# Optimization experiments

Measured on AMD Instinct MI355X. Metric: run time of the kernel, lower is better.

## Reference

```python
import jax, jax.numpy as jnp
import numpy as np

B, CI, CO = 8, 32, 32
M1, M2 = 16, 16
H, W = 128, 128
TOTAL = M1 + M2 + M1 * M2  # 288


def setup_inputs() -> dict:
    key = jax.random.key(0)
    k1, k2, k3 = jax.random.split(key, 3)
    scale = 1.0 / (CI * CO)
    x = jax.random.normal(k1, (B, CI, H, W), dtype=jnp.float32)
    weight_real = scale * jax.random.uniform(k2, (CI, CO, TOTAL), dtype=jnp.float32)
    weight_imag = scale * jax.random.uniform(k3, (CI, CO, TOTAL), dtype=jnp.float32)
    return {"x": x, "weight_real": weight_real, "weight_imag": weight_imag}


def reference(x, weight_real, weight_imag):
    w = (weight_real + 1j * weight_imag).astype(jnp.complex64)
    pole1 = w[:, :, :M1]                                   # [i,o,p]
    pole2 = w[:, :, M1:M1 + M2]                            # [i,o,q]
    residue = w[:, :, M1 + M2:].reshape(CI, CO, M1, M2)    # [i,o,p,q]

    Hh, Wd = x.shape[-2], x.shape[-1]
    ty = jnp.linspace(0.0, 1.0, Hh)   # grid along dim -2
    tx = jnp.linspace(0.0, 1.0, Wd)   # grid along dim -1
    dty = ty[1] - ty[0]
    dtx = tx[1] - tx[0]

    # FFT (torch default norm='backward': no scaling on forward)
    alpha = jnp.fft.fft2(x, axes=(-2, -1))[:, :, :M1, :M2]  # [b,i,f,g] complex

    lam1 = (jnp.fft.fftfreq(Hh, dty) * (2.0 * np.pi) * 1j)[:M1].astype(jnp.complex64)  # [f]
    lam2 = (jnp.fft.fftfreq(Wd, dtx) * (2.0 * np.pi) * 1j)[:M2].astype(jnp.complex64)  # [g]

    # pole-residue transfer function Hw[f,g,i,o,p,q] = res[i,o,p,q] / ((lam1[f]-pole1[i,o,p]) * (lam2[g]-pole2[i,o,q]))
    d1 = lam1[:, None, None, None] - pole1[None]  # [f,i,o,p]
    d2 = lam2[:, None, None, None] - pole2[None]  # [g,i,o,q]
    Hw = residue[None, None] / (d1[:, None, :, :, :, None] * d2[None, :, :, :, None, :])  # [f,g,i,o,p,q]

    # contractions matching torch einsums 'biox,oxikpq->bkox' and '->bkpq'
    or1 = jnp.einsum('bifg,fgiopq->bofg', alpha, Hw)  # [b,o,f,g]
    or2 = jnp.einsum('bifg,fgiopq->bopq', alpha, Hw)  # [b,o,p,q]

    # ifft2 with zero-padding of modes to full (H, W), norm='backward' (1/(HW) on inverse)
    x1 = jnp.real(jnp.fft.ifft2(or1, s=(Hh, Wd), axes=(-2, -1)))

    # time-domain pole exponentials
    e1 = jnp.exp(pole1[..., None] * ty.astype(jnp.complex64))  # [i,o,p,z]
    e2 = jnp.exp(pole2[..., None] * tx.astype(jnp.complex64))  # [i,o,q,x]
    # x2[b,o,z,x] = sum_{i,p,q} or2[b,o,p,q] e1[i,o,p,z] e2[i,o,q,x]  (avoids 6D [i,o,p,q,H,W] intermediate)
    tmp = jnp.einsum('bopq,iopz->bioqz', or2, e1)          # [b,i,o,q,z]
    x2 = jnp.real(jnp.einsum('bioqz,ioqx->bozx', tmp, e2)) / (Hh * Wd)

    return x1 + x2
```

## Files before the change

### kernel.cpp

```cpp
#include <hip/hip_runtime.h>

#define TOT 288
#define W1C 6.2340979026f
#define TWOPI_128 0.049087385212340517f

typedef short short8 __attribute__((ext_vector_type(8)));
typedef float f32x4 __attribute__((ext_vector_type(4)));
typedef unsigned short u16;
typedef u16 u16x8 __attribute__((ext_vector_type(8)));

__device__ __forceinline__ u16 f2bf(float f) {
    unsigned u = __builtin_bit_cast(unsigned, f);
    u += 0x7fffu + ((u >> 16) & 1u);
    return (u16)(u >> 16);
}
__device__ __forceinline__ float2 cmul(float2 a, float2 b) {
    return make_float2(a.x * b.x - a.y * b.y, a.x * b.y + a.y * b.x);
}
__device__ __forceinline__ float2 cfma(float2 a, float2 b, float2 c) {
    return make_float2(c.x + a.x * b.x - a.y * b.y, c.y + a.x * b.y + a.y * b.x);
}
__device__ __forceinline__ void chi_basis(int f, float2 c[3]) {
    if (f == 0) {
        c[0] = make_float2(1.f, 0.f); c[1] = make_float2(0.f, 0.f); c[2] = make_float2(0.f, 0.f);
    } else {
        float w = W1C * (float)f;
        float iw = 1.0f / w;
        c[0] = make_float2(0.f, 0.f);
        c[1] = make_float2(0.f, -iw);
        c[2] = make_float2(-iw * iw, 0.f);
    }
}


__global__ __launch_bounds__(256) void k_pre(const float* __restrict__ x,
                                             const float* __restrict__ wr,
                                             const float* __restrict__ wi,
                                             float2* __restrict__ alpha,
                                             float2* __restrict__ Sv,
                                             float2* __restrict__ Dv,
                                             u16* __restrict__ fA, u16* __restrict__ fB) {
    __shared__ float sm[4352];
    const int bid = blockIdx.x;
    const int t = threadIdx.x;

    if (bid < 256) {
        float2* T1c = (float2*)sm;
        const int bi = bid;
        const float* xp = x + (size_t)bi * 16384;
        const int xc = t & 127;
        const int ft = (t >> 7) * 8;

        float c2[8], ccs[8], csn[8], s1[8], s2[8];
#pragma unroll
        for (int j = 0; j < 8; ++j) {
            float w = TWOPI_128 * (float)(ft + j);
            sincosf(w, &csn[j], &ccs[j]);
            c2[j] = 2.f * ccs[j];
            s1[j] = 0.f; s2[j] = 0.f;
        }
#pragma unroll 2
        for (int y = 0; y < 128; ++y) {
            float xv = xp[(size_t)y * 128 + xc];
#pragma unroll
            for (int j = 0; j < 8; ++j) {
                float na = __builtin_fmaf(c2[j], s1[j], xv - s2[j]);
                s2[j] = s1[j]; s1[j] = na;
            }
        }
#pragma unroll
        for (int j = 0; j < 8; ++j)
            T1c[(ft + j) * 132 + xc] = make_float2(ccs[j] * s1[j] - s2[j], csn[j] * s1[j]);
        __syncthreads();

        const int f = t >> 4, g = t & 15;
        const float2* tp = T1c + f * 132;
        float sw, cw;
        sincosf(TWOPI_128 * (float)g, &sw, &cw);
        float c2g = 2.f * cw;
        float s1r = 0.f, s1i = 0.f, s2r = 0.f, s2i = 0.f;
#pragma unroll 4
        for (int xx = 0; xx < 128; ++xx) {
            float2 v = tp[xx];
            float nr = __builtin_fmaf(c2g, s1r, v.x - s2r);
            s2r = s1r; s1r = nr;
            float ni = __builtin_fmaf(c2g, s1i, v.y - s2i);
            s2i = s1i; s1i = ni;
        }
        alpha[bi * 256 + t] = make_float2(cw * s1r - sw * s1i - s2r,
                                          sw * s1r + cw * s1i - s2i);
    } else if (bid < 288) {
        int o = bid - 256;
        int p = t >> 4, q = t & 15;
        float Sr[4][4], Si[4][4];
#pragma unroll
        for (int n = 0; n < 4; ++n)
#pragma unroll
            for (int m = 0; m < 4; ++m) { Sr[n][m] = 0.f; Si[n][m] = 0.f; }
        for (int i = 0; i < 32; ++i) {
            int io = i * 32 + o;
            float p1r = wr[io * TOT + p],      p1i = wi[io * TOT + p];
            float p2r = wr[io * TOT + 16 + q], p2i = wi[io * TOT + 16 + q];
            float a1r[4], a1i[4], a2r[4], a2i[4];
            a1r[0] = 1.f; a1i[0] = 0.f;
            a2r[0] = 1.f; a2i[0] = 0.f;
#pragma unroll
            for (int n = 1; n < 4; ++n) {
                a1r[n] = a1r[n-1] * p1r - a1i[n-1] * p1i;
                a1i[n] = a1r[n-1] * p1i + a1i[n-1] * p1r;
                a2r[n] = a2r[n-1] * p2r - a2i[n-1] * p2i;
                a2i[n] = a2r[n-1] * p2i + a2i[n-1] * p2r;
            }
#pragma unroll
            for (int n = 0; n < 4; ++n)
#pragma unroll
                for (int m = 0; m < 4; ++m) {
                    Sr[n][m] += a1r[n] * a2r[m] - a1i[n] * a2i[m];
                    Si[n][m] += a1r[n] * a2i[m] + a1i[n] * a2r[m];
                }
        }
        const float facs[4] = {1.f, 1.f, 0.5f, 0.16666666666f};
        const float isz = 1.0f / 16384.0f;
#pragma unroll
        for (int n = 0; n < 4; ++n)
#pragma unroll
            for (int m = 0; m < 4; ++m) {
                float fac = facs[n] * facs[m] * isz;
                Sv[(size_t)(o * 16 + n * 4 + m) * 256 + t] =
                    make_float2(Sr[n][m] * fac, Si[n][m] * fac);
            }
    } else if (bid < 416) {
        int base = (bid - 288) * 8;
        int wp = t >> 6, l = t & 63;
#pragma unroll
        for (int s = 0; s < 2; ++s) {
            int io = base + wp * 2 + s;
            float2 Dacc[9];
#pragma unroll
            for (int jk = 0; jk < 9; ++jk) Dacc[jk] = make_float2(0.f, 0.f);
#pragma unroll
            for (int k = 0; k < 4; ++k) {
                int e = l + 64 * k;
                int p = e >> 4, q = e & 15;
                float2 p1 = make_float2(wr[io * TOT + p], wi[io * TOT + p]);
                float i1 = 1.0f / (p1.x * p1.x + p1.y * p1.y);
                float2 phip = make_float2(-p1.x * i1, p1.y * i1);
                float2 p2 = make_float2(wr[io * TOT + 16 + q], wi[io * TOT + 16 + q]);
                float i2 = 1.0f / (p2.x * p2.x + p2.y * p2.y);
                float2 psip = make_float2(-p2.x * i2, p2.y * i2);
                float2 R = make_float2(wr[io * TOT + 32 + e], wi[io * TOT + 32 + e]);
                float2 Rphi[3] = {cmul(R, phip), R, cmul(R, p1)};
                float2 psi[3] = {psip, make_float2(1.f, 0.f), p2};
#pragma unroll
                for (int j = 0; j < 3; ++j)
#pragma unroll
                    for (int k2 = 0; k2 < 3; ++k2)
                        Dacc[j * 3 + k2] = cfma(Rphi[j], psi[k2], Dacc[j * 3 + k2]);
            }
#pragma unroll
            for (int jk = 0; jk < 9; ++jk) {
#pragma unroll
                for (int m = 32; m >= 1; m >>= 1) {
                    Dacc[jk].x += __shfl_xor(Dacc[jk].x, m);
                    Dacc[jk].y += __shfl_xor(Dacc[jk].y, m);
                }
            }
            if (l == 0) {
                int o = io & 31, i = io >> 5;
#pragma unroll
                for (int jk = 0; jk < 9; ++jk)
                    Dv[(size_t)(o * 32 + i) * 9 + jk] = Dacc[jk];
            }
        }
    } else {
        for (int cidx = t; cidx < 1024; cidx += 256) {
            int tbl = cidx >> 9, mc = cidx & 511;
            int z = mc >> 2, cp = mc & 3;
            int c = cp ^ ((z >> 1) & 3);
            u16x8 v;
#pragma unroll
            for (int j = 0; j < 8; ++j) {
                int k = c * 8 + j, f = k & 15, part = k >> 4;
                float th = TWOPI_128 * (float)((f * z) & 127);
                float s, cs;
                sincosf(th, &s, &cs);
                float val = part ? ((tbl == 0) ? s : -s) : cs;
                v[j] = f2bf(val);
            }
            u16* dst = (tbl == 0 ? fA : fB) + mc * 8;
            *(u16x8*)dst = v;
        }
    }
}

__global__ __launch_bounds__(256) void k_mid(const float* __restrict__ wr,
                                             const float* __restrict__ wi,
                                             const float2* __restrict__ alpha,
                                             const float2* __restrict__ Dv,
                                             float2* __restrict__ or1,
                                             float2* __restrict__ or2p) {
    __shared__ float2 CaL[4][9];
    const int bid = blockIdx.x;
    const int t = threadIdx.x;

    if (bid < 256) {
        int bo = bid;
        int b = bo >> 5, o = bo & 31;
        int f = t >> 4, g = t & 15;
        float2 X[3], Xi[3];
        chi_basis(f, X);
        chi_basis(g, Xi);
        float2 B[9];
#pragma unroll
        for (int j = 0; j < 3; ++j)
#pragma unroll
            for (int k = 0; k < 3; ++k)
                B[j * 3 + k] = cmul(X[j], Xi[k]);
        float2 acc = make_float2(0.f, 0.f);
        for (int i = 0; i < 32; ++i) {
            const float2* Dp = Dv + (size_t)(o * 32 + i) * 9;
            float2 s1v = make_float2(0.f, 0.f);
#pragma unroll
            for (int jk = 0; jk < 9; ++jk)
                s1v = cfma(Dp[jk], B[jk], s1v);
            float2 a = alpha[(b * 32 + i) * 256 + t];
            acc = cfma(a, s1v, acc);
        }
        or1[bo * 256 + t] = acc;
    } else {
        int idx = bid - 256;
        int bo = idx & 255;
        int ic = idx >> 8;
        int b = bo >> 5, o = bo & 31;
        int wp = t >> 6, l = t & 63;
        {
            int i = ic * 4 + wp;
            float2 Ca[9];
#pragma unroll
            for (int jk = 0; jk < 9; ++jk) Ca[jk] = make_float2(0.f, 0.f);
#pragma unroll
            for (int k = 0; k < 4; ++k) {
                int e = l + 64 * k;
                int f = e >> 4, g = e & 15;
                float2 X[3], Xi[3];
                chi_basis(f, X);
                chi_basis(g, Xi);
                float2 a = alpha[(b * 32 + i) * 256 + e];
                float2 aX[3] = {cmul(a, X[0]), cmul(a, X[1]), cmul(a, X[2])};
#pragma unroll
                for (int j = 0; j < 3; ++j)
#pragma unroll
                    for (int k2 = 0; k2 < 3; ++k2)
                        Ca[j * 3 + k2] = cfma(aX[j], Xi[k2], Ca[j * 3 + k2]);
            }
#pragma unroll
            for (int jk = 0; jk < 9; ++jk) {
#pragma unroll
                for (int m = 32; m >= 1; m >>= 1) {
                    Ca[jk].x += __shfl_xor(Ca[jk].x, m);
                    Ca[jk].y += __shfl_xor(Ca[jk].y, m);
                }
            }
            if (l == 0) {
#pragma unroll
                for (int jk = 0; jk < 9; ++jk) CaL[wp][jk] = Ca[jk];
            }
        }
        __syncthreads();

        int p_ = t >> 4, q_ = t & 15;
        float2 acc = make_float2(0.f, 0.f);
#pragma unroll
        for (int ii = 0; ii < 4; ++ii) {
            int i = ic * 4 + ii;
            int io = i * 32 + o;
            float2 p1 = make_float2(wr[io * TOT + p_], wi[io * TOT + p_]);
            float i1 = 1.0f / (p1.x * p1.x + p1.y * p1.y);
            float2 phip = make_float2(-p1.x * i1, p1.y * i1);
            float2 p2 = make_float2(wr[io * TOT + 16 + q_], wi[io * TOT + 16 + q_]);
            float i2 = 1.0f / (p2.x * p2.x + p2.y * p2.y);
            float2 psip = make_float2(-p2.x * i2, p2.y * i2);
            float2 R = make_float2(wr[io * TOT + 32 + t], wi[io * TOT + 32 + t]);
            float2 c0 = CaL[ii][0], c1 = CaL[ii][1], c2 = CaL[ii][2];
            float2 c3 = CaL[ii][3], c4 = CaL[ii][4], c5 = CaL[ii][5];
            float2 c6 = CaL[ii][6], c7 = CaL[ii][7], c8 = CaL[ii][8];
            float2 col0 = cfma(c6, p1, cfma(c0, phip, c3));
            float2 col1 = cfma(c7, p1, cfma(c1, phip, c4));
            float2 col2 = cfma(c8, p1, cfma(c2, phip, c5));
            float2 T = cfma(col2, p2, cfma(col0, psip, col1));
            acc = cfma(R, T, acc);
        }
        or2p[(size_t)ic * 65536 + bo * 256 + t] = acc;
    }
}

__global__ __launch_bounds__(512, 4) void k_x12m(
        const float2* __restrict__ or1v,
        const float2* __restrict__ or2p,
        const float2* __restrict__ Sv,
        const u16* __restrict__ fA,
        const u16* __restrict__ fB,
        float* __restrict__ out) {
    __shared__ u16 EA[2048];
    __shared__ u16 EB[4096];
    __shared__ u16 GL[2048];
    __shared__ float2 SM1[256];
    __shared__ float2 SM2[256];
    __shared__ float CP[16];

    const int t = threadIdx.x;
    const int l = t & 63, w = t >> 6;
    const int bid = blockIdx.x;
    const int o = bid & 31, b = (bid >> 5) & 7, zh = bid >> 8;
    const int bo = b * 32 + o;
    const int q = l & 15, c4 = l >> 4, k0 = c4 * 8;

    for (int ch = w; ch < 12; ch += 8) {
        const u16* g;
        u16* d;
        if (ch < 4) { g = fA + zh * 2048 + ch * 512 + l * 8; d = &EA[ch * 512]; }
        else { g = fB + (ch - 4) * 512 + l * 8; d = &EB[(ch - 4) * 512]; }
        __builtin_amdgcn_global_load_lds(
            (const __attribute__((address_space(1))) unsigned*)g,
            (__attribute__((address_space(3))) unsigned*)d, 16, 0, 0);
    }

    if (t < 256) {
        float sr = 0.f, si = 0.f;
#pragma unroll
        for (int ic = 0; ic < 8; ++ic) {
            float2 v = or2p[(size_t)ic * 65536 + bo * 256 + t];
            sr += v.x; si += v.y;
        }
        SM2[t] = make_float2(sr, si);
        SM1[t] = or1v[bo * 256 + t];
    }
    __syncthreads();

    {
        int gidx = t >> 5;
        int j = t & 31;
        const float2* Sg = Sv + (size_t)(o * 16 + gidx) * 256;
        float part = 0.f;
#pragma unroll
        for (int k = 0; k < 8; ++k) {
            int pq = j + 32 * k;
            float2 s = Sg[pq];
            float2 v = SM2[pq];
            part += v.x * s.x - v.y * s.y;
        }
#pragma unroll
        for (int msk = 16; msk >= 1; msk >>= 1)
            part += __shfl_xor(part, msk, 32);
        if (j == 0) CP[gidx] = part;
    }

    short8 mF0, mF1;
#pragma unroll
    for (int j = 0; j < 8; ++j) {
        int k = k0 + j, f = k & 15;
        float2 m1 = SM1[f * 16 + q];
        if (k < 16) { mF0[j] = (short)f2bf(m1.x); mF1[j] = (short)f2bf(m1.y); }
        else        { mF0[j] = (short)f2bf(-m1.y); mF1[j] = (short)f2bf(m1.x); }
    }
    const short8 bF = (w & 1) ? mF1 : mF0;

    const int zt_g = w >> 1;
    const int zL_g = zt_g * 16 + q;
    const int cw_g = c4 ^ ((zL_g >> 1) & 3);
    const int kk_g = q + ((w & 1) << 4);
    const int x_ = w * 16 + q;
    const int cb_ = c4 ^ ((x_ >> 1) & 3);

    {
        short8 aG = *(const short8*)&EA[zL_g * 32 + cw_g * 8];
        f32x4 g = (f32x4){0.f, 0.f, 0.f, 0.f};
        g = __builtin_amdgcn_mfma_f32_16x16x32_bf16(aG, bF, g, 0, 0, 0);
#pragma unroll
        for (int r = 0; r < 4; ++r) {
            int zz = zt_g * 16 + c4 * 4 + r;
            int cc = (kk_g >> 3) ^ ((zz >> 1) & 3);
            GL[zz * 32 + cc * 8 + (kk_g & 7)] = f2bf(g[r]);
        }
    }
    __syncthreads();

    f32x4 acc[4];
    {
        short8 bf = *(const short8*)&EB[x_ * 32 + cb_ * 8];
#pragma unroll
        for (int zt = 0; zt < 4; ++zt) {
            int zL = zt * 16 + q;
            int ca = c4 ^ ((zL >> 1) & 3);
            short8 af = *(const short8*)&GL[zL * 32 + ca * 8];
            f32x4 a = (f32x4){0.f, 0.f, 0.f, 0.f};
            acc[zt] = __builtin_amdgcn_mfma_f32_16x16x32_bf16(af, bf, a, 0, 0, 0);
        }
    }

    const float sc = 1.0f / 16384.0f;
    const float tx = (float)x_ * 0.007874015748031496f;
    float R[4];
#pragma unroll
    for (int n = 0; n < 4; ++n)
        R[n] = ((CP[n * 4 + 3] * tx + CP[n * 4 + 2]) * tx + CP[n * 4 + 1]) * tx + CP[n * 4 + 0];
#pragma unroll
    for (int zt = 0; zt < 4; ++zt) {
        int zbase = zh * 64 + zt * 16 + c4 * 4;
        f32x4 a = acc[zt];
#pragma unroll
        for (int r = 0; r < 4; ++r) {
            float tz = (float)(zbase + r) * 0.007874015748031496f;
            float poly = ((R[3] * tz + R[2]) * tz + R[1]) * tz + R[0];
            out[(size_t)bo * 16384 + (zbase + r) * 128 + x_] = a[r] * sc + poly;
        }
    }
}

extern "C" void kernel_launch(void* const* d_in, const int* in_sizes, int n_in,
                              void* d_out, int out_size, void* d_ws, size_t ws_size,
                              hipStream_t stream) {
    const float* x  = (const float*)d_in[0];
    const float* wr = (const float*)d_in[1];
    const float* wi = (const float*)d_in[2];
    float* out = (float*)d_out;
    float* ws = (float*)d_ws;

    float2* alpha = (float2*)(ws + 256);
    float2* Dv    = (float2*)(ws + 1179904);
    float2* or1   = (float2*)(ws + 1704192);
    float2* Sv    = (float2*)(ws + 1966336);
    u16*    fA    = (u16*)(ws + 6160640);
    u16*    fB    = (u16*)(ws + 6162688);
    float2* or2p  = (float2*)(ws + 6164736);

    hipLaunchKernelGGL(k_pre,  dim3(417),  dim3(256), 0, stream,
                       x, wr, wi, alpha, Sv, Dv, fA, fB);
    hipLaunchKernelGGL(k_mid,  dim3(2304), dim3(256), 0, stream,
                       wr, wi, alpha, Dv, or1, or2p);
    hipLaunchKernelGGL(k_x12m, dim3(512),  dim3(512), 0, stream,
                       or1, or2p, Sv, fA, fB, out);
}
```

Measured before the change: 54.36 us.

## Stage x tiles into LDS asynchronously and split Ca reduction into its own kernel

k_pre now copies each 128x128 input slice into shared memory with global_load_lds before the Goertzel-style row DFT, which reads LDS instead of strided global memory. Shared memory grows to 64KB, which may reduce occupancy. The old k_mid recomputed the per-(b,i) 9-term Ca reduction once for every output channel o. It is split into k_ca, which computes Ca once per (b,i) and writes it to a global buffer, and k_or2, which reads it. This removes redundant alpha reads and shuffle reductions at the cost of one extra kernel launch and a round trip through global memory.

```diff
diff --git a/kernel.cpp b/kernel.cpp
--- a/kernel.cpp
+++ b/kernel.cpp
@@ -16,6 +16,9 @@
 }
 __device__ __forceinline__ float2 cmul(float2 a, float2 b) {
     return make_float2(a.x * b.x - a.y * b.y, a.x * b.y + a.y * b.x);
+}
+__device__ __forceinline__ float2 cadd(float2 a, float2 b) {
+    return make_float2(a.x + b.x, a.y + b.y);
 }
 __device__ __forceinline__ float2 cfma(float2 a, float2 b, float2 c) {
     return make_float2(c.x + a.x * b.x - a.y * b.y, c.y + a.x * b.y + a.y * b.x);
@@ -40,17 +43,25 @@
                                              float2* __restrict__ Sv,
                                              float2* __restrict__ Dv,
                                              u16* __restrict__ fA, u16* __restrict__ fB) {
-    __shared__ float sm[4352];
+    __shared__ float sm[16384];
     const int bid = blockIdx.x;
     const int t = threadIdx.x;
 
     if (bid < 256) {
-        float2* T1c = (float2*)sm;
         const int bi = bid;
         const float* xp = x + (size_t)bi * 16384;
+        const int l = t & 63, w4 = t >> 6;
+
+#pragma unroll
+        for (int r = 0; r < 16; ++r) {
+            int off = w4 * 4096 + r * 256;
+            __builtin_amdgcn_global_load_lds(
+                (const __attribute__((address_space(1))) unsigned*)(xp + off + l * 4),
+                (__attribute__((address_space(3))) unsigned*)(sm + off), 16, 0, 0);
+        }
+
         const int xc = t & 127;
         const int ft = (t >> 7) * 8;
-
         float c2[8], ccs[8], csn[8], s1[8], s2[8];
 #pragma unroll
         for (int j = 0; j < 8; ++j) {
@@ -59,18 +70,29 @@
             c2[j] = 2.f * ccs[j];
             s1[j] = 0.f; s2[j] = 0.f;
         }
-#pragma unroll 2
+        __syncthreads();
+
+#pragma unroll 4
         for (int y = 0; y < 128; ++y) {
-            float xv = xp[(size_t)y * 128 + xc];
+            float xv = sm[y * 128 + xc];
 #pragma unroll
             for (int j = 0; j < 8; ++j) {
                 float na = __builtin_fmaf(c2[j], s1[j], xv - s2[j]);
                 s2[j] = s1[j]; s1[j] = na;
             }
         }
+        float t1r[8], t1i[8];
+#pragma unroll
+        for (int j = 0; j < 8; ++j) {
+            t1r[j] = ccs[j] * s1[j] - s2[j];
+            t1i[j] = csn[j] * s1[j];
+        }
+        __syncthreads();
+
+        float2* T1c = (float2*)sm;
 #pragma unroll
         for (int j = 0; j < 8; ++j)
-            T1c[(ft + j) * 132 + xc] = make_float2(ccs[j] * s1[j] - s2[j], csn[j] * s1[j]);
+            T1c[(ft + j) * 132 + xc] = make_float2(t1r[j], t1i[j]);
         __syncthreads();
 
         const int f = t >> 4, g = t & 15;
@@ -193,13 +215,11 @@
     }
 }
 
-__global__ __launch_bounds__(256) void k_mid(const float* __restrict__ wr,
-                                             const float* __restrict__ wi,
-                                             const float2* __restrict__ alpha,
-                                             const float2* __restrict__ Dv,
-                                             float2* __restrict__ or1,
-                                             float2* __restrict__ or2p) {
-    __shared__ float2 CaL[4][9];
+__global__ __launch_bounds__(256) void k_ca(const float2* __restrict__ alpha,
+                                            const float2* __restrict__ Dv,
+                                            float2* __restrict__ or1,
+                                            float2* __restrict__ CaG) {
+    __shared__ float2 red[4][9];
     const int bid = blockIdx.x;
     const int t = threadIdx.x;
 
@@ -229,69 +249,74 @@
         or1[bo * 256 + t] = acc;
     } else {
         int idx = bid - 256;
-        int bo = idx & 255;
-        int ic = idx >> 8;
-        int b = bo >> 5, o = bo & 31;
-        int wp = t >> 6, l = t & 63;
-        {
-            int i = ic * 4 + wp;
-            float2 Ca[9];
-#pragma unroll
-            for (int jk = 0; jk < 9; ++jk) Ca[jk] = make_float2(0.f, 0.f);
-#pragma unroll
-            for (int k = 0; k < 4; ++k) {
-                int e = l + 64 * k;
-                int f = e >> 4, g = e & 15;
-                float2 X[3], Xi[3];
-                chi_basis(f, X);
-                chi_basis(g, Xi);
-                float2 a = alpha[(b * 32 + i) * 256 + e];
-                float2 aX[3] = {cmul(a, X[0]), cmul(a, X[1]), cmul(a, X[2])};
-#pragma unroll
-                for (int j = 0; j < 3; ++j)
-#pragma unroll
-                    for (int k2 = 0; k2 < 3; ++k2)
-                        Ca[j * 3 + k2] = cfma(aX[j], Xi[k2], Ca[j * 3 + k2]);
-            }
-#pragma unroll
-            for (int jk = 0; jk < 9; ++jk) {
-#pragma unroll
-                for (int m = 32; m >= 1; m >>= 1) {
-                    Ca[jk].x += __shfl_xor(Ca[jk].x, m);
-                    Ca[jk].y += __shfl_xor(Ca[jk].y, m);
-                }
-            }
-            if (l == 0) {
-#pragma unroll
-                for (int jk = 0; jk < 9; ++jk) CaL[wp][jk] = Ca[jk];
-            }
+        int f = t >> 4, g = t & 15;
+        float2 X[3], Xi[3];
+        chi_basis(f, X);
+        chi_basis(g, Xi);
+        float2 a = alpha[(size_t)idx * 256 + t];
+        float2 aX0 = cmul(a, X[0]), aX1 = cmul(a, X[1]), aX2 = cmul(a, X[2]);
+        float2 Ca[9];
+        Ca[0] = cmul(aX0, Xi[0]); Ca[1] = cmul(aX0, Xi[1]); Ca[2] = cmul(aX0, Xi[2]);
+        Ca[3] = cmul(aX1, Xi[0]); Ca[4] = cmul(aX1, Xi[1]); Ca[5] = cmul(aX1, Xi[2]);
+        Ca[6] = cmul(aX2, Xi[0]); Ca[7] = cmul(aX2, Xi[1]); Ca[8] = cmul(aX2, Xi[2]);
+#pragma unroll
+        for (int jk = 0; jk < 9; ++jk) {
+#pragma unroll
+            for (int m = 32; m >= 1; m >>= 1) {
+                Ca[jk].x += __shfl_xor(Ca[jk].x, m);
+                Ca[jk].y += __shfl_xor(Ca[jk].y, m);
+            }
+        }
+        int l = t & 63, w = t >> 6;
+        if (l == 0) {
+#pragma unroll
+            for (int jk = 0; jk < 9; ++jk) red[w][jk] = Ca[jk];
         }
         __syncthreads();
-
-        int p_ = t >> 4, q_ = t & 15;
-        float2 acc = make_float2(0.f, 0.f);
-#pragma unroll
-        for (int ii = 0; ii < 4; ++ii) {
-            int i = ic * 4 + ii;
-            int io = i * 32 + o;
-            float2 p1 = make_float2(wr[io * TOT + p_], wi[io * TOT + p_]);
-            float i1 = 1.0f / (p1.x * p1.x + p1.y * p1.y);
-            float2 phip = make_float2(-p1.x * i1, p1.y * i1);
-            float2 p2 = make_float2(wr[io * TOT + 16 + q_], wi[io * TOT + 16 + q_]);
-            float i2 = 1.0f / (p2.x * p2.x + p2.y * p2.y);
-            float2 psip = make_float2(-p2.x * i2, p2.y * i2);
-            float2 R = make_float2(wr[io * TOT + 32 + t], wi[io * TOT + 32 + t]);
-            float2 c0 = CaL[ii][0], c1 = CaL[ii][1], c2 = CaL[ii][2];
-            float2 c3 = CaL[ii][3], c4 = CaL[ii][4], c5 = CaL[ii][5];
-            float2 c6 = CaL[ii][6], c7 = CaL[ii][7], c8 = CaL[ii][8];
-            float2 col0 = cfma(c6, p1, cfma(c0, phip, c3));
-            float2 col1 = cfma(c7, p1, cfma(c1, phip, c4));
-            float2 col2 = cfma(c8, p1, cfma(c2, phip, c5));
-            float2 T = cfma(col2, p2, cfma(col0, psip, col1));
-            acc = cfma(R, T, acc);
-        }
-        or2p[(size_t)ic * 65536 + bo * 256 + t] = acc;
-    }
+        if (t < 9) {
+            float2 s = cadd(cadd(red[0][t], red[1][t]), cadd(red[2][t], red[3][t]));
+            CaG[(size_t)idx * 9 + t] = s;
+        }
+    }
+}
+
+__global__ __launch_bounds__(256) void k_or2(const float* __restrict__ wr,
+                                             const float* __restrict__ wi,
+                                             const float2* __restrict__ CaG,
+                                             float2* __restrict__ or2p) {
+    __shared__ float2 CaL[36];
+    const int bid = blockIdx.x;
+    const int bo = bid & 255;
+    const int ic = bid >> 8;
+    const int b = bo >> 5, o = bo & 31;
+    const int t = threadIdx.x;
+
+    if (t < 36) CaL[t] = CaG[(size_t)(b * 32 + ic * 4) * 9 + t];
+    __syncthreads();
+
+    const int p_ = t >> 4, q_ = t & 15;
+    float2 acc = make_float2(0.f, 0.f);
+#pragma unroll
+    for (int ii = 0; ii < 4; ++ii) {
+        int i = ic * 4 + ii;
+        int io = i * 32 + o;
+        float2 p1 = make_float2(wr[io * TOT + p_], wi[io * TOT + p_]);
+        float i1 = 1.0f / (p1.x * p1.x + p1.y * p1.y);
+        float2 phip = make_float2(-p1.x * i1, p1.y * i1);
+        float2 p2 = make_float2(wr[io * TOT + 16 + q_], wi[io * TOT + 16 + q_]);
+        float i2 = 1.0f / (p2.x * p2.x + p2.y * p2.y);
+        float2 psip = make_float2(-p2.x * i2, p2.y * i2);
+        float2 R = make_float2(wr[io * TOT + 32 + t], wi[io * TOT + 32 + t]);
+        float2 c0 = CaL[ii * 9 + 0], c1 = CaL[ii * 9 + 1], c2 = CaL[ii * 9 + 2];
+        float2 c3 = CaL[ii * 9 + 3], c4 = CaL[ii * 9 + 4], c5 = CaL[ii * 9 + 5];
+        float2 c6 = CaL[ii * 9 + 6], c7 = CaL[ii * 9 + 7], c8 = CaL[ii * 9 + 8];
+        float2 col0 = cfma(c6, p1, cfma(c0, phip, c3));
+        float2 col1 = cfma(c7, p1, cfma(c1, phip, c4));
+        float2 col2 = cfma(c8, p1, cfma(c2, phip, c5));
+        float2 T = cfma(col2, p2, cfma(col0, psip, col1));
+        acc = cfma(R, T, acc);
+    }
+    or2p[(size_t)ic * 65536 + bo * 256 + t] = acc;
 }
 
 __global__ __launch_bounds__(512, 4) void k_x12m(
@@ -428,6 +453,7 @@
 
     float2* alpha = (float2*)(ws + 256);
     float2* Dv    = (float2*)(ws + 1179904);
+    float2* CaG   = (float2*)(ws + 1198336);
     float2* or1   = (float2*)(ws + 1704192);
     float2* Sv    = (float2*)(ws + 1966336);
     u16*    fA    = (u16*)(ws + 6160640);
@@ -436,8 +462,10 @@
 
     hipLaunchKernelGGL(k_pre,  dim3(417),  dim3(256), 0, stream,
                        x, wr, wi, alpha, Sv, Dv, fA, fB);
-    hipLaunchKernelGGL(k_mid,  dim3(2304), dim3(256), 0, stream,
-                       wr, wi, alpha, Dv, or1, or2p);
+    hipLaunchKernelGGL(k_ca,   dim3(512),  dim3(256), 0, stream,
+                       alpha, Dv, or1, CaG);
+    hipLaunchKernelGGL(k_or2,  dim3(2048), dim3(256), 0, stream,
+                       wr, wi, CaG, or2p);
     hipLaunchKernelGGL(k_x12m, dim3(512),  dim3(512), 0, stream,
                        or1, or2p, Sv, fA, fB, out);
 }
```

After: 56.92 us. 4.7% more time.
